# Kernel tuning notes

Measured on AMD Instinct MI355X. Metric: run time of the kernel, lower is better.

Reference implementation:

```python
import jax, jax.numpy as jnp
import numpy as np

BS, L, D = 2048, 32, 768
KS = 5  # gaussian kernel size
EPS = 1e-5


def layer_norm(x, g, b):
    m = x.mean(-1, keepdims=True)
    var = ((x - m) ** 2).mean(-1, keepdims=True)
    return (x - m) * jax.lax.rsqrt(var + EPS) * g + b


def setup_inputs() -> dict:
    key = jax.random.key(0)
    ks = jax.random.split(key, 12)
    s = 0.02
    return {
        "v": jax.random.normal(ks[0], (BS, L, D), jnp.float32),
        "qa": jax.random.normal(ks[1], (BS, D), jnp.float32),
        # v_proj: LayerNorm -> Linear(D,D) -> GELU
        "vp_lng": jnp.ones((D,), jnp.float32),
        "vp_lnb": jnp.zeros((D,), jnp.float32),
        "vp_w": jax.random.normal(ks[2], (D, D), jnp.float32) * s,
        "vp_b": jnp.zeros((D,), jnp.float32),
        # qa_proj: LayerNorm -> Linear(D,D) -> GELU
        "qp_lng": jnp.ones((D,), jnp.float32),
        "qp_lnb": jnp.zeros((D,), jnp.float32),
        "qp_w": jax.random.normal(ks[3], (D, D), jnp.float32) * s,
        "qp_b": jnp.zeros((D,), jnp.float32),
        # grounding: LayerNorm -> Linear(D,D/2) -> GELU -> Linear(D/2,1) -> Softmax(dim=-2)
        "g_lng": jnp.ones((D,), jnp.float32),
        "g_lnb": jnp.zeros((D,), jnp.float32),
        "g_w1": jax.random.normal(ks[4], (D, D // 2), jnp.float32) * s,
        "g_b1": jnp.zeros((D // 2,), jnp.float32),
        "g_w2": jax.random.normal(ks[5], (D // 2, 1), jnp.float32) * s,
        "g_b2": jnp.zeros((1,), jnp.float32),
        # adaptive gaussian filter sigma (scalar parameter, initial 1.0)
        "sigma": jnp.array(1.0, jnp.float32),
    }


def reference(v, qa, vp_lng, vp_lnb, vp_w, vp_b, qp_lng, qp_lnb, qp_w, qp_b,
              g_lng, g_lnb, g_w1, g_b1, g_w2, g_b2, sigma):
    bs, length = v.shape[0], v.shape[1]
    # projections (exact erf GELU, matching torch nn.GELU default)
    v_p = jax.nn.gelu(layer_norm(v, vp_lng, vp_lnb) @ vp_w + vp_b, approximate=False)
    qa_p = jax.nn.gelu(layer_norm(qa, qp_lng, qp_lnb) @ qp_w + qp_b, approximate=False)
    # gate = tanh(v @ qa) : [bs, L, 1]
    gate = jnp.tanh(jnp.einsum('bld,bd->bl', v_p, qa_p))[..., None]
    # grounding head -> softmax over frames
    h = layer_norm(v_p * gate, g_lng, g_lnb)
    h = jax.nn.gelu(h @ g_w1 + g_b1, approximate=False)
    logits = h @ g_w2 + g_b2                      # [bs, L, 1]
    ori_key = jax.nn.softmax(logits, axis=1)[..., 0]  # [bs, L]
    # adaptive gaussian smoothing (depthwise conv1d, symmetric 5-tap kernel) + softmax
    xk = jnp.arange(KS, dtype=jnp.float32) - KS // 2
    kern = jnp.exp(-0.5 * (xk / sigma) ** 2)
    kern = kern / kern.sum()
    xp = jnp.pad(ori_key, ((0, 0), (KS // 2, KS // 2)))
    taps = jnp.stack([xp[:, k:k + length] for k in range(KS)], axis=0)  # [KS, bs, L]
    smoothed = jnp.einsum('k,kbl->bl', kern, taps)
    key_gs = jax.nn.softmax(smoothed, axis=1)         # [bs, L]
    # find_best_interval_v2, vectorized: among windows of size {1,3,5} that
    # contain the (first) argmax frame, pick the window with highest prob-sum;
    # ties resolve to smallest window then earliest start (strict > in loop ==
    # first occurrence of the max in (w, start) order == jnp.argmax semantics).
    pmax = jnp.argmax(key_gs, axis=1)                 # [bs]
    cum = jnp.pad(jnp.cumsum(key_gs, axis=1), ((0, 0), (1, 0)))
    scores_all, starts_all, ends_all = [], [], []
    for w in (1, 3, 5):
        s = jnp.arange(length - w + 1)
        sums = cum[:, s + w] - cum[:, s]              # sliding window sums
        contains = (pmax[:, None] >= s[None, :]) & (pmax[:, None] < s[None, :] + w)
        scores_all.append(jnp.where(contains, sums, -jnp.inf))
        starts_all.append(s)
        ends_all.append(s + w)                        # NOTE: exclusive end stored, as in original
    scores = jnp.concatenate(scores_all, axis=1)
    starts = jnp.concatenate(starts_all)
    ends = jnp.concatenate(ends_all)
    idx = jnp.argmax(scores, axis=1)
    st = starts[idx]
    en = ends[idx]
    max_indices = jnp.stack([st, en], axis=1)         # [bs, 2]
    rng = jnp.arange(length)
    mask = (rng[None, :] >= st[:, None]) & (rng[None, :] <= en[:, None])
    start_time = st.astype(jnp.float32) / 31.0
    end_time = en.astype(jnp.float32) / 31.0
    return key_gs, max_indices, start_time, end_time, mask, ori_key
```

## Files before the change

kernel.cpp:

```cpp
#include <hip/hip_runtime.h>
#include <math.h>
#include <stdint.h>


#define DEV __device__ __forceinline__

typedef __attribute__((ext_vector_type(8))) short short8v;
typedef __attribute__((ext_vector_type(4))) float f32x4;

constexpr int KDIM  = 768;
constexpr int CHUNK = 32768;

constexpr int OFF_KG   = 0;
constexpr int OFF_MI   = 65536;
constexpr int OFF_ST   = 69632;
constexpr int OFF_ET   = 71680;
constexpr int OFF_MASK = 73728;
constexpr int OFF_ORI  = 139264;

DEV float wave_sum(float v) { for (int o = 32; o; o >>= 1) v += __shfl_xor(v, o); return v; }
DEV float wave_max(float v) { for (int o = 32; o; o >>= 1) v = fmaxf(v, __shfl_xor(v, o)); return v; }

DEV float gelu_fast(float x) {
    float z = x * 0.70710678118654752f;
    float s = fabsf(z);
    float t = __builtin_amdgcn_rcpf(fmaf(0.3275911f, s, 1.0f));
    float p = t * fmaf(t, fmaf(t, fmaf(t, fmaf(t, 1.061405429f, -1.453152027f),
                                       1.421413741f), -0.284496736f), 0.254829592f);
    float e = __expf(-s * s);
    float er = copysignf(1.0f - p * e, z);
    return 0.5f * x * (1.0f + er);
}

DEV short f2bf(float x) {
    uint32_t u = __builtin_bit_cast(uint32_t, x);
    u = u + 0x7fffu + ((u >> 16) & 1u);
    return (short)(u >> 16);
}
DEV float bf2f(short b) {
    uint32_t u = ((uint32_t)(uint16_t)b) << 16;
    return __builtin_bit_cast(float, u);
}
DEV float asf(uint32_t u) { return __builtin_bit_cast(float, u); }

DEV void gl_lds16(const void* g, void* l) {
    __builtin_amdgcn_global_load_lds(
        (const __attribute__((address_space(1))) uint32_t*)g,
        (__attribute__((address_space(3))) uint32_t*)l, 16, 0, 0);
}

__global__ __launch_bounds__(256)
void prep_A1(const float* __restrict__ X, const float* __restrict__ g,
             const float* __restrict__ b, short* __restrict__ Ah, short* __restrict__ Al)
{
    int w = threadIdx.x >> 6, lane = threadIdx.x & 63;
    int row = blockIdx.x * 4 + w;
    const float4* xr = (const float4*)(X + (size_t)row * KDIM);
    float4 xv[3]; float s = 0.f, ss = 0.f;
#pragma unroll
    for (int i = 0; i < 3; ++i) {
        xv[i] = xr[lane + i * 64];
        s  += xv[i].x + xv[i].y + xv[i].z + xv[i].w;
        ss += xv[i].x * xv[i].x + xv[i].y * xv[i].y + xv[i].z * xv[i].z + xv[i].w * xv[i].w;
    }
    s = wave_sum(s); ss = wave_sum(ss);
    float m = s * (1.f / 768.f), var = ss * (1.f / 768.f) - m * m;
    float sa = rsqrtf(var + 1e-5f), ta = -m * sa;
#pragma unroll
    for (int i = 0; i < 3; ++i) {
        int idx = lane + i * 64;
        float4 gv = ((const float4*)g)[idx];
        float4 bv = ((const float4*)b)[idx];
        float a0 = fmaf(fmaf(xv[i].x, sa, ta), gv.x, bv.x);
        float a1 = fmaf(fmaf(xv[i].y, sa, ta), gv.y, bv.y);
        float a2 = fmaf(fmaf(xv[i].z, sa, ta), gv.z, bv.z);
        float a3 = fmaf(fmaf(xv[i].w, sa, ta), gv.w, bv.w);
        short h0 = f2bf(a0), h1 = f2bf(a1), h2 = f2bf(a2), h3 = f2bf(a3);
        ushort4 hv, lv;
        hv.x = (uint16_t)h0; hv.y = (uint16_t)h1; hv.z = (uint16_t)h2; hv.w = (uint16_t)h3;
        lv.x = (uint16_t)f2bf(a0 - bf2f(h0)); lv.y = (uint16_t)f2bf(a1 - bf2f(h1));
        lv.z = (uint16_t)f2bf(a2 - bf2f(h2)); lv.w = (uint16_t)f2bf(a3 - bf2f(h3));
        ((ushort4*)(Ah + (size_t)row * KDIM))[idx] = hv;
        ((ushort4*)(Al + (size_t)row * KDIM))[idx] = lv;
    }
}

__global__ __launch_bounds__(256)
void prep_W(const float* __restrict__ W, const float* __restrict__ scale,
            short* __restrict__ Bh, short* __restrict__ Bl, int N)
{
    __shared__ float t[32][33];
    int bx = blockIdx.x, by = blockIdx.y;
    int lx = threadIdx.x & 31, ly = threadIdx.x >> 5;
#pragma unroll
    for (int r = 0; r < 32; r += 8)
        t[ly + r][lx] = W[(size_t)(by * 32 + ly + r) * N + bx * 32 + lx];
    __syncthreads();
    float sc = scale ? scale[by * 32 + lx] : 1.0f;
#pragma unroll
    for (int r = 0; r < 32; r += 8) {
        float v = t[lx][ly + r] * sc;
        short hi = f2bf(v);
        size_t o = (size_t)(bx * 32 + ly + r) * KDIM + by * 32 + lx;
        Bh[o] = hi;
        Bl[o] = f2bf(v - bf2f(hi));
    }
}

__global__ __launch_bounds__(256)
void colsums(const float* __restrict__ W1, const float* __restrict__ g2,
             const float* __restrict__ lb2, const float* __restrict__ b1,
             float* __restrict__ c1, float* __restrict__ c2)
{
    int w = threadIdx.x >> 6, lane = threadIdx.x & 63;
    int n = blockIdx.x * 4 + w;
    float s1 = 0.f, s2 = 0.f;
    for (int k = lane; k < 768; k += 64) {
        float wv = W1[(size_t)k * 384 + n];
        s1 += g2[k] * wv;
        s2 += lb2[k] * wv;
    }
    s1 = wave_sum(s1); s2 = wave_sum(s2);
    if (lane == 0) { c1[n] = s1; c2[n] = b1[n] + s2; }
}

__global__ __launch_bounds__(256)
void stats2(const float* __restrict__ sums, float2* __restrict__ st2, int chunk_off)
{
    int r = chunk_off + blockIdx.x * 256 + threadIdx.x;
    float s = 0.f, ss = 0.f, d = 0.f;
#pragma unroll
    for (int p = 0; p < 8; ++p) {
        s  += sums[(size_t)(0 * 8 + p) * 65536 + r];
        ss += sums[(size_t)(1 * 8 + p) * 65536 + r];
        d  += sums[(size_t)(2 * 8 + p) * 65536 + r];
    }
    float gate = tanhf(d);
    float m = s * (1.f / 768.f), var = ss * (1.f / 768.f) - m * m;
    float den = rsqrtf(gate * gate * var + 1e-5f);
    st2[r] = make_float2(gate * den, -gate * m * den);
}

#define VMW(N_) asm volatile("s_waitcnt vmcnt(" #N_ ")" ::: "memory")
#define SCB __builtin_amdgcn_sched_barrier(0)

#define STG(G_, KT_) gl_lds16(sp[G_] + (KT_) * 32,                            \
    lds + (((KT_) & 1) ? BUFSZ : 0) + (G_) * 4096 + toff)

#define STGA10(KT_) do { STG(0, KT_); STG(1, KT_); STG(2, KT_); STG(3, KT_);  \
    STG(4, KT_); STG(5, KT_); STG(6, KT_); STG(7, KT_); STG(8, KT_);          \
    STG(9, KT_); } while (0)

#define RDA(dst, BOFF) do { _Pragma("unroll")                                 \
    for (int mf = 0; mf < 4; ++mf) {                                          \
        int rA = wm * 64 + mf * 16 + lr;                                      \
        dst[mf] = *(const short8v*)(bb + (BOFF) + rA * 64 +                   \
                                    ((lh ^ ((rA >> 1) & 3)) << 4));           \
    } } while (0)

#define RDB(dst, BOFF) do { _Pragma("unroll")                                 \
    for (int nf = 0; nf < 6; ++nf) {                                          \
        int rB = wn * 96 + nf * 16 + lr;                                      \
        dst[nf] = *(const short8v*)(bb + (BOFF) + rB * 64 +                   \
                                    ((lh ^ ((rB >> 1) & 3)) << 4));           \
    } } while (0)

#define BODY(KT_, NL_) do {                                                   \
    if (NL_) { STGA10((KT_) + 1); }                                           \
    SCB;                                                                      \
    if (NL_) { VMW(10); } else { VMW(0); }                                    \
    SCB;                                                                      \
    __builtin_amdgcn_s_barrier();                \
    const char* bb = lds + (((KT_) & 1) ? BUFSZ : 0);                         \
    RDA(ah, 0); RDA(al, 8192); RDB(bh, 16384); RDB(bl, 28672);                \
    asm volatile("s_waitcnt lgkmcnt(0)" ::: "memory");                        \
    SCB;                                                                      \
    __builtin_amdgcn_s_barrier();                     \
    __builtin_amdgcn_s_setprio(1);                                            \
    _Pragma("unroll")                                                         \
    for (int mf = 0; mf < 4; ++mf)                                            \
        _Pragma("unroll")                                                     \
        for (int nf = 0; nf < 6; ++nf) {                                      \
            acc[mf][nf] = __builtin_amdgcn_mfma_f32_16x16x32_bf16(            \
                ah[mf], bh[nf], acc[mf][nf], 0, 0, 0);                        \
            acc[mf][nf] = __builtin_amdgcn_mfma_f32_16x16x32_bf16(            \
                ah[mf], bl[nf], acc[mf][nf], 0, 0, 0);                        \
            acc[mf][nf] = __builtin_amdgcn_mfma_f32_16x16x32_bf16(            \
                al[mf], bh[nf], acc[mf][nf], 0, 0, 0);                        \
        }                                                                     \
    __builtin_amdgcn_s_setprio(0);                                            \
    SCB;                                                                      \
} while (0)

template<int MODE>
__global__ __launch_bounds__(256, 2)
void gemm8(const short* __restrict__ Ah_g, const short* __restrict__ Al_g,
           const short* __restrict__ Bh_g, const short* __restrict__ Bl_g,
           const float* __restrict__ bias,
           short* __restrict__ Oh, short* __restrict__ Ol,
           const float* __restrict__ qa_p, float* __restrict__ sums,
           const float2* __restrict__ st2, const float* __restrict__ c1,
           const float* __restrict__ c2, const float* __restrict__ w2,
           float* __restrict__ partials, int chunk_off)
{
    constexpr int BUFSZ = 40960;
    extern __shared__ __align__(16) char lds[];

    const int t = threadIdx.x;
    const int w = t >> 6, lane = t & 63;
    const int lr = lane & 15, lh = lane >> 4;
    const int wm = w >> 1, wn = w & 1;

    const int gx = gridDim.x, nwg = gx * gridDim.y;
    int bidx = blockIdx.y * gx + blockIdx.x;
    int wid = (bidx & 7) * (nwg >> 3) + (bidx >> 3);
    const int bx = wid % gx, by = wid / gx;
    const int row0 = by * 128, col0 = bx * 192;

    const int r_ = t >> 2, c_ = t & 3;
    const int swz_ = (c_ ^ ((r_ >> 1) & 3)) << 3;
    const int toff = t * 16;
    const short* sp[10];
    sp[0] = Ah_g + (size_t)(row0 + r_)       * KDIM + swz_;
    sp[1] = Ah_g + (size_t)(row0 + 64 + r_)  * KDIM + swz_;
    sp[2] = Al_g + (size_t)(row0 + r_)       * KDIM + swz_;
    sp[3] = Al_g + (size_t)(row0 + 64 + r_)  * KDIM + swz_;
    sp[4] = Bh_g + (size_t)(col0 + r_)       * KDIM + swz_;
    sp[5] = Bh_g + (size_t)(col0 + 64 + r_)  * KDIM + swz_;
    sp[6] = Bh_g + (size_t)(col0 + 128 + r_) * KDIM + swz_;
    sp[7] = Bl_g + (size_t)(col0 + r_)       * KDIM + swz_;
    sp[8] = Bl_g + (size_t)(col0 + 64 + r_)  * KDIM + swz_;
    sp[9] = Bl_g + (size_t)(col0 + 128 + r_) * KDIM + swz_;

    f32x4 acc[4][6] = {};
    short8v ah[4], al[4], bh[6], bl[6];

    STGA10(0);
    SCB;

    for (int kt = 0; kt < 24; kt += 2) {
        BODY(kt,     true);
        BODY(kt + 1, (kt + 1 < 23));
    }

    if (MODE == 0) {
        __syncthreads();
        float* qal = (float*)lds;
        int bbase = (chunk_off >> 5) + (row0 >> 5);
        for (int j = t; j < 768; j += 256)
            qal[j] = qa_p[(size_t)(bbase + j / 192) * 768 + col0 + (j % 192)];
        __syncthreads();
#pragma unroll
        for (int mf = 0; mf < 4; ++mf) {
            const int bp = wm * 2 + (mf >> 1);
#pragma unroll
            for (int q = 0; q < 4; ++q) {
                int m = row0 + wm * 64 + mf * 16 + lh * 4 + q;
                float s = 0.f, ssq = 0.f, d = 0.f;
#pragma unroll
                for (int nf = 0; nf < 6; ++nf) {
                    int ncol = wn * 96 + nf * 16 + lr;
                    int n = col0 + ncol;
                    float gv = gelu_fast(acc[mf][nf][q] + bias[n]);
                    uint32_t u  = __builtin_bit_cast(uint32_t, gv);
                    uint32_t hb = u & 0xffff0000u;
                    float rem   = gv - asf(hb);
                    Oh[(size_t)m * 768 + n] = (short)(hb >> 16);
                    Ol[(size_t)m * 768 + n] = f2bf(rem);
                    s += gv; ssq += gv * gv; d += gv * qal[bp * 192 + ncol];
                }
                for (int o = 1; o < 16; o <<= 1) {
                    s += __shfl_xor(s, o); ssq += __shfl_xor(ssq, o); d += __shfl_xor(d, o);
                }
                if (lr == 0) {
                    int gr = chunk_off + m;
                    int pc = bx * 2 + wn;
                    sums[(size_t)(0 * 8 + pc) * 65536 + gr] = s;
                    sums[(size_t)(1 * 8 + pc) * 65536 + gr] = ssq;
                    sums[(size_t)(2 * 8 + pc) * 65536 + gr] = d;
                }
            }
        }
    } else {
        float c1v[6], c2v[6], wv[6];
#pragma unroll
        for (int nf = 0; nf < 6; ++nf) {
            int n = col0 + wn * 96 + nf * 16 + lr;
            c1v[nf] = c1[n]; c2v[nf] = c2[n]; wv[nf] = w2[n];
        }
        float rs[4][4] = {};
#pragma unroll
        for (int mf = 0; mf < 4; ++mf)
#pragma unroll
            for (int q = 0; q < 4; ++q) {
                int gm = chunk_off + row0 + wm * 64 + mf * 16 + lh * 4 + q;
                float2 st = st2[gm];
#pragma unroll
                for (int nf = 0; nf < 6; ++nf) {
                    float h = fmaf(st.x, acc[mf][nf][q], fmaf(st.y, c1v[nf], c2v[nf]));
                    rs[mf][q] += gelu_fast(h) * wv[nf];
                }
            }
#pragma unroll
        for (int mf = 0; mf < 4; ++mf)
#pragma unroll
            for (int q = 0; q < 4; ++q) {
                float vv = rs[mf][q];
                vv += __shfl_xor(vv, 1); vv += __shfl_xor(vv, 2);
                vv += __shfl_xor(vv, 4); vv += __shfl_xor(vv, 8);
                if (lr == 0) {
                    int gm = chunk_off + row0 + wm * 64 + mf * 16 + lh * 4 + q;
                    partials[(size_t)(bx * 2 + wn) * 65536 + gm] = vv;
                }
            }
    }
}

constexpr int BKF = 16;
__global__ __launch_bounds__(256)
void rowstats(const float* __restrict__ X, float2* __restrict__ st, int M)
{
    int wave = threadIdx.x >> 6, lane = threadIdx.x & 63;
    int row = blockIdx.x * 4 + wave;
    if (row >= M) return;
    const float4* xr = reinterpret_cast<const float4*>(X + (size_t)row * KDIM);
    float s = 0.f, ss = 0.f;
#pragma unroll
    for (int i = 0; i < 3; ++i) {
        float4 v = xr[lane + i * 64];
        s  += v.x + v.y + v.z + v.w;
        ss += v.x * v.x + v.y * v.y + v.z * v.z + v.w * v.w;
    }
    s = wave_sum(s); ss = wave_sum(ss);
    if (lane == 0) {
        float m = s * (1.0f / 768.0f);
        float var = ss * (1.0f / 768.0f) - m * m;
        float rstd = rsqrtf(var + 1e-5f);
        st[row] = make_float2(rstd, -m * rstd);
    }
}

template<int BM, int BN, int TM, int TN>
__global__ __launch_bounds__(256)
void gemm_fused(const float* __restrict__ X, const float2* __restrict__ st,
                const float* __restrict__ gw, const float* __restrict__ gb,
                const float* __restrict__ W, const float* __restrict__ bias,
                float* __restrict__ out, int M, int N)
{
    static_assert((BM / TM) * (BN / TN) == 256, "256 threads");
    __shared__ float As[BKF][BM];
    __shared__ float Bs[BKF][BN];
    const int t = threadIdx.x;
    constexpr int TXN = BN / TN;
    const int tx = t % TXN;
    const int ty = t / TXN;
    const int row0 = blockIdx.y * BM;
    const int col0 = blockIdx.x * BN;
    float acc[TM][TN] = {};
    constexpr int A_IT = BM * BKF / 4 / 256;
    constexpr int B_IT = BKF * BN / 4 / 256;
    for (int k0 = 0; k0 < KDIM; k0 += BKF) {
#pragma unroll
        for (int i = 0; i < A_IT; ++i) {
            int idx = t + i * 256;
            int r = idx >> 2;
            int c = (idx & 3) << 2;
            float4 xv = *reinterpret_cast<const float4*>(X + (size_t)(row0 + r) * KDIM + k0 + c);
            float2 s = st[row0 + r];
            float4 gv = *reinterpret_cast<const float4*>(gw + k0 + c);
            float4 bv = *reinterpret_cast<const float4*>(gb + k0 + c);
            As[c + 0][r] = fmaf(fmaf(xv.x, s.x, s.y), gv.x, bv.x);
            As[c + 1][r] = fmaf(fmaf(xv.y, s.x, s.y), gv.y, bv.y);
            As[c + 2][r] = fmaf(fmaf(xv.z, s.x, s.y), gv.z, bv.z);
            As[c + 3][r] = fmaf(fmaf(xv.w, s.x, s.y), gv.w, bv.w);
        }
#pragma unroll
        for (int i = 0; i < B_IT; ++i) {
            int idx = t + i * 256;
            int r = idx / (BN / 4);
            int c = (idx % (BN / 4)) << 2;
            *reinterpret_cast<float4*>(&Bs[r][c]) =
                *reinterpret_cast<const float4*>(W + (size_t)(k0 + r) * N + col0 + c);
        }
        __syncthreads();
#pragma unroll
        for (int kk = 0; kk < BKF; ++kk) {
            float a[TM], b[TN];
#pragma unroll
            for (int i = 0; i < TM; i += 4)
                *reinterpret_cast<float4*>(&a[i]) = *reinterpret_cast<const float4*>(&As[kk][ty * TM + i]);
#pragma unroll
            for (int j = 0; j < TN; j += 4)
                *reinterpret_cast<float4*>(&b[j]) = *reinterpret_cast<const float4*>(&Bs[kk][tx * TN + j]);
#pragma unroll
            for (int i = 0; i < TM; ++i)
#pragma unroll
                for (int j = 0; j < TN; ++j)
                    acc[i][j] = fmaf(a[i], b[j], acc[i][j]);
        }
        __syncthreads();
    }
#pragma unroll
    for (int i = 0; i < TM; ++i) {
        size_t row = row0 + ty * TM + i;
#pragma unroll
        for (int j = 0; j < TN; j += 4) {
            int col = col0 + tx * TN + j;
            float4 o;
            o.x = gelu_fast(acc[i][j + 0] + bias[col + 0]);
            o.y = gelu_fast(acc[i][j + 1] + bias[col + 1]);
            o.z = gelu_fast(acc[i][j + 2] + bias[col + 2]);
            o.w = gelu_fast(acc[i][j + 3] + bias[col + 3]);
            *reinterpret_cast<float4*>(out + row * N + col) = o;
        }
    }
}

__global__ __launch_bounds__(64)
void head_kernel(const float* __restrict__ partials, const float* __restrict__ b2,
                 const float* __restrict__ sigma_p, float* __restrict__ out)
{
    int b = blockIdx.x, lane = threadIdx.x;
    __shared__ float ok[36];
    __shared__ float kg[32];
    __shared__ int sel[2];

    if (lane < 36) ok[lane] = 0.f;
    __syncthreads();

    float x = -3.4e38f;
    if (lane < 32) {
        int row = b * 32 + lane;
        x = b2[0];
#pragma unroll
        for (int p = 0; p < 4; ++p) x += partials[(size_t)p * 65536 + row];
    }
    float mx = wave_max(x);
    float e = (lane < 32) ? expf(x - mx) : 0.f;
    float sum = wave_sum(e);
    float ori = e / sum;
    if (lane < 32) {
        out[OFF_ORI + b * 32 + lane] = ori;
        ok[lane + 2] = ori;
    }
    __syncthreads();

    float sg = sigma_p[0];
    float kern[5]; float ks = 0.f;
#pragma unroll
    for (int k = 0; k < 5; ++k) { float xx = (float)(k - 2) / sg; kern[k] = expf(-0.5f * xx * xx); ks += kern[k]; }
    float sm = -3.4e38f;
    if (lane < 32) {
        sm = 0.f;
#pragma unroll
        for (int k = 0; k < 5; ++k) sm += (kern[k] / ks) * ok[lane + k];
    }
    float mx2 = wave_max(sm);
    float e2 = (lane < 32) ? expf(sm - mx2) : 0.f;
    float sum2 = wave_sum(e2);
    float kgv = e2 / sum2;
    if (lane < 32) {
        out[OFF_KG + b * 32 + lane] = kgv;
        kg[lane] = kgv;
    }
    __syncthreads();

    if (lane == 0) {
        int pm = 0; float bv = kg[0];
        for (int i = 1; i < 32; ++i) if (kg[i] > bv) { bv = kg[i]; pm = i; }
        float cum[33]; cum[0] = 0.f;
        for (int i = 0; i < 32; ++i) cum[i + 1] = cum[i] + kg[i];
        float bs = -3.4e38f; int bst = 0, ben = 0;
        const int wsz[3] = {1, 3, 5};
        for (int wi = 0; wi < 3; ++wi) {
            int w = wsz[wi];
            for (int s = 0; s + w <= 32; ++s) {
                if (pm >= s && pm < s + w) {
                    float sc = cum[s + w] - cum[s];
                    if (sc > bs) { bs = sc; bst = s; ben = s + w; }
                }
            }
        }
        out[OFF_MI + b * 2 + 0] = (float)bst;
        out[OFF_MI + b * 2 + 1] = (float)ben;
        out[OFF_ST + b] = (float)bst / 31.0f;
        out[OFF_ET + b] = (float)ben / 31.0f;
        sel[0] = bst; sel[1] = ben;
    }
    __syncthreads();
    if (lane < 32)
        out[OFF_MASK + b * 32 + lane] = (lane >= sel[0] && lane <= sel[1]) ? 1.0f : 0.0f;
}

extern "C" void kernel_launch(void* const* d_in, const int* in_sizes, int n_in,
                              void* d_out, int out_size, void* d_ws, size_t ws_size,
                              hipStream_t stream)
{
    const float* v      = (const float*)d_in[0];
    const float* qa     = (const float*)d_in[1];
    const float* vp_lng = (const float*)d_in[2];
    const float* vp_lnb = (const float*)d_in[3];
    const float* vp_w   = (const float*)d_in[4];
    const float* vp_b   = (const float*)d_in[5];
    const float* qp_lng = (const float*)d_in[6];
    const float* qp_lnb = (const float*)d_in[7];
    const float* qp_w   = (const float*)d_in[8];
    const float* qp_b   = (const float*)d_in[9];
    const float* g_lng  = (const float*)d_in[10];
    const float* g_lnb  = (const float*)d_in[11];
    const float* g_w1   = (const float*)d_in[12];
    const float* g_b1   = (const float*)d_in[13];
    const float* g_w2   = (const float*)d_in[14];
    const float* g_b2   = (const float*)d_in[15];
    const float* sigma  = (const float*)d_in[16];
    float* outf = (float*)d_out;

    short* A1h = (short*)d_ws;
    short* A1l = A1h + (size_t)CHUNK * KDIM;
    short* vph = A1l + (size_t)CHUNK * KDIM;
    short* vpl = vph + (size_t)CHUNK * KDIM;
    short* B1h = vpl + (size_t)CHUNK * KDIM;
    short* B1l = B1h + 768 * KDIM;
    short* B2h = B1l + 768 * KDIM;
    short* B2l = B2h + 384 * KDIM;
    float* qa_p = (float*)(B2l + 384 * KDIM);
    float* st_qa = qa_p + 2048 * KDIM;
    float* partials = st_qa + 4096;
    float* sums = partials + 4 * 65536;
    float2* st2 = (float2*)(sums + 24 * 65536);
    float* c1 = (float*)(st2 + 65536);
    float* c2 = c1 + 384;

    rowstats<<<512, 256, 0, stream>>>(qa, (float2*)st_qa, 2048);
    gemm_fused<64, 64, 4, 4><<<dim3(12, 32), 256, 0, stream>>>(
        qa, (const float2*)st_qa, qp_lng, qp_lnb, qp_w, qp_b, qa_p, 2048, 768);

    prep_W<<<dim3(24, 24), 256, 0, stream>>>(vp_w, nullptr, B1h, B1l, 768);
    prep_W<<<dim3(12, 24), 256, 0, stream>>>(g_w1, g_lng, B2h, B2l, 384);
    colsums<<<96, 256, 0, stream>>>(g_w1, g_lng, g_lnb, g_b1, c1, c2);

    constexpr int LDS8 = 81920;

    for (int c = 0; c < 65536; c += CHUNK) {
        prep_A1<<<CHUNK / 4, 256, 0, stream>>>(v + (size_t)c * KDIM, vp_lng, vp_lnb, A1h, A1l);
        gemm8<0><<<dim3(4, CHUNK / 128), 256, LDS8, stream>>>(
            A1h, A1l, B1h, B1l, vp_b, vph, vpl, qa_p, sums,
            nullptr, nullptr, nullptr, nullptr, nullptr, c);
        stats2<<<CHUNK / 256, 256, 0, stream>>>(sums, st2, c);
        gemm8<1><<<dim3(2, CHUNK / 128), 256, LDS8, stream>>>(
            vph, vpl, B2h, B2l, nullptr, nullptr, nullptr, nullptr, nullptr,
            (const float2*)st2, c1, c2, g_w2, partials, c);
    }

    head_kernel<<<2048, 64, 0, stream>>>(partials, g_b2, sigma, outf);
}
```

Baseline: 517.3 us.

## Interleave bf16 hi/lo split of A operands into packed 32-bit words

Stores the activations' bf16 high and low halves together as one packed uint32 per element, replacing two separate short arrays. This applies to the LayerNorm prep output and to the first GEMM's GELU output that feeds the second GEMM. The GEMM staging now loads A rows from a single interleaved buffer with a new XOR swizzle, then unpacks hi and lo fragments in registers with shifts and masks before the MFMAs. The intent is fewer, wider global stores and contiguous A loads. The cost is extra ALU unpack work in the inner loop and a changed LDS bank pattern.

```diff
diff --git a/kernel.cpp b/kernel.cpp
--- a/kernel.cpp
+++ b/kernel.cpp
@@ -7,6 +7,7 @@
 
 typedef __attribute__((ext_vector_type(8))) short short8v;
 typedef __attribute__((ext_vector_type(4))) float f32x4;
+typedef __attribute__((ext_vector_type(4))) uint32_t u32x4;
 
 constexpr int KDIM  = 768;
 constexpr int CHUNK = 32768;
@@ -43,15 +44,36 @@
 }
 DEV float asf(uint32_t u) { return __builtin_bit_cast(float, u); }
 
+DEV uint32_t packhl(float x) {
+    uint32_t u  = __builtin_bit_cast(uint32_t, x);
+    uint32_t hb = u & 0xffff0000u;
+    float rem   = x - asf(hb);
+    return hb | (uint32_t)(uint16_t)f2bf(rem);
+}
+
 DEV void gl_lds16(const void* g, void* l) {
     __builtin_amdgcn_global_load_lds(
         (const __attribute__((address_space(1))) uint32_t*)g,
         (__attribute__((address_space(3))) uint32_t*)l, 16, 0, 0);
 }
 
+DEV void unpack8(u32x4 p0, u32x4 p1, short8v& hi, short8v& lo) {
+    u32x4 h, l;
+    h.x = (p0.x >> 16) | (p0.y & 0xffff0000u);
+    h.y = (p0.z >> 16) | (p0.w & 0xffff0000u);
+    h.z = (p1.x >> 16) | (p1.y & 0xffff0000u);
+    h.w = (p1.z >> 16) | (p1.w & 0xffff0000u);
+    l.x = (p0.x & 0xffffu) | (p0.y << 16);
+    l.y = (p0.z & 0xffffu) | (p0.w << 16);
+    l.z = (p1.x & 0xffffu) | (p1.y << 16);
+    l.w = (p1.z & 0xffffu) | (p1.w << 16);
+    hi = __builtin_bit_cast(short8v, h);
+    lo = __builtin_bit_cast(short8v, l);
+}
+
 __global__ __launch_bounds__(256)
 void prep_A1(const float* __restrict__ X, const float* __restrict__ g,
-             const float* __restrict__ b, short* __restrict__ Ah, short* __restrict__ Al)
+             const float* __restrict__ b, uint32_t* __restrict__ Ap)
 {
     int w = threadIdx.x >> 6, lane = threadIdx.x & 63;
     int row = blockIdx.x * 4 + w;
@@ -71,17 +93,12 @@
         int idx = lane + i * 64;
         float4 gv = ((const float4*)g)[idx];
         float4 bv = ((const float4*)b)[idx];
-        float a0 = fmaf(fmaf(xv[i].x, sa, ta), gv.x, bv.x);
-        float a1 = fmaf(fmaf(xv[i].y, sa, ta), gv.y, bv.y);
-        float a2 = fmaf(fmaf(xv[i].z, sa, ta), gv.z, bv.z);
-        float a3 = fmaf(fmaf(xv[i].w, sa, ta), gv.w, bv.w);
-        short h0 = f2bf(a0), h1 = f2bf(a1), h2 = f2bf(a2), h3 = f2bf(a3);
-        ushort4 hv, lv;
-        hv.x = (uint16_t)h0; hv.y = (uint16_t)h1; hv.z = (uint16_t)h2; hv.w = (uint16_t)h3;
-        lv.x = (uint16_t)f2bf(a0 - bf2f(h0)); lv.y = (uint16_t)f2bf(a1 - bf2f(h1));
-        lv.z = (uint16_t)f2bf(a2 - bf2f(h2)); lv.w = (uint16_t)f2bf(a3 - bf2f(h3));
-        ((ushort4*)(Ah + (size_t)row * KDIM))[idx] = hv;
-        ((ushort4*)(Al + (size_t)row * KDIM))[idx] = lv;
+        uint4 ov;
+        ov.x = packhl(fmaf(fmaf(xv[i].x, sa, ta), gv.x, bv.x));
+        ov.y = packhl(fmaf(fmaf(xv[i].y, sa, ta), gv.y, bv.y));
+        ov.z = packhl(fmaf(fmaf(xv[i].z, sa, ta), gv.z, bv.z));
+        ov.w = packhl(fmaf(fmaf(xv[i].w, sa, ta), gv.w, bv.w));
+        ((uint4*)(Ap + (size_t)row * KDIM))[idx] = ov;
     }
 }
 
@@ -144,18 +161,23 @@
 #define VMW(N_) asm volatile("s_waitcnt vmcnt(" #N_ ")" ::: "memory")
 #define SCB __builtin_amdgcn_sched_barrier(0)
 
-#define STG(G_, KT_) gl_lds16(sp[G_] + (KT_) * 32,                            \
-    lds + (((KT_) & 1) ? BUFSZ : 0) + (G_) * 4096 + toff)
-
-#define STGA10(KT_) do { STG(0, KT_); STG(1, KT_); STG(2, KT_); STG(3, KT_);  \
-    STG(4, KT_); STG(5, KT_); STG(6, KT_); STG(7, KT_); STG(8, KT_);          \
-    STG(9, KT_); } while (0)
-
-#define RDA(dst, BOFF) do { _Pragma("unroll")                                 \
+#define STGA(U_, KT_) gl_lds16(spA[U_] + (KT_) * 32,                          \
+    lds + (((KT_) & 1) ? BUFSZ : 0) + (U_) * 4096 + toff)
+#define STGB(J_, KT_) gl_lds16(spB[J_] + (KT_) * 32,                          \
+    lds + (((KT_) & 1) ? BUFSZ : 0) + 16384 + (J_) * 4096 + toff)
+
+#define STGALL(KT_) do { STGA(0, KT_); STGA(1, KT_); STGA(2, KT_);            \
+    STGA(3, KT_); STGB(0, KT_); STGB(1, KT_); STGB(2, KT_); STGB(3, KT_);     \
+    STGB(4, KT_); STGB(5, KT_); } while (0)
+
+#define RDAP do { _Pragma("unroll")                                           \
     for (int mf = 0; mf < 4; ++mf) {                                          \
         int rA = wm * 64 + mf * 16 + lr;                                      \
-        dst[mf] = *(const short8v*)(bb + (BOFF) + rA * 64 +                   \
-                                    ((lh ^ ((rA >> 1) & 3)) << 4));           \
+        const char* pr = bb + rA * 128;                                       \
+        int x_ = rA & 7;                                                      \
+        u32x4 p0 = *(const u32x4*)(pr + (((2 * lh) ^ x_) << 4));              \
+        u32x4 p1 = *(const u32x4*)(pr + (((2 * lh + 1) ^ x_) << 4));          \
+        unpack8(p0, p1, ah[mf], al[mf]);                                      \
     } } while (0)
 
 #define RDB(dst, BOFF) do { _Pragma("unroll")                                 \
@@ -166,13 +188,13 @@
     } } while (0)
 
 #define BODY(KT_, NL_) do {                                                   \
-    if (NL_) { STGA10((KT_) + 1); }                                           \
+    if (NL_) { STGALL((KT_) + 1); }                                           \
     SCB;                                                                      \
     if (NL_) { VMW(10); } else { VMW(0); }                                    \
     SCB;                                                                      \
     __builtin_amdgcn_s_barrier();                \
     const char* bb = lds + (((KT_) & 1) ? BUFSZ : 0);                         \
-    RDA(ah, 0); RDA(al, 8192); RDB(bh, 16384); RDB(bl, 28672);                \
+    RDAP; RDB(bh, 16384); RDB(bl, 28672);                                     \
     asm volatile("s_waitcnt lgkmcnt(0)" ::: "memory");                        \
     SCB;                                                                      \
     __builtin_amdgcn_s_barrier();                     \
@@ -194,10 +216,9 @@
 
 template<int MODE>
 __global__ __launch_bounds__(256, 2)
-void gemm8(const short* __restrict__ Ah_g, const short* __restrict__ Al_g,
+void gemm8(const uint32_t* __restrict__ Ap_g,
            const short* __restrict__ Bh_g, const short* __restrict__ Bl_g,
-           const float* __restrict__ bias,
-           short* __restrict__ Oh, short* __restrict__ Ol,
+           const float* __restrict__ bias, uint32_t* __restrict__ O_hl,
            const float* __restrict__ qa_p, float* __restrict__ sums,
            const float2* __restrict__ st2, const float* __restrict__ c1,
            const float* __restrict__ c2, const float* __restrict__ w2,
@@ -217,25 +238,28 @@
     const int bx = wid % gx, by = wid / gx;
     const int row0 = by * 128, col0 = bx * 192;
 
-    const int r_ = t >> 2, c_ = t & 3;
-    const int swz_ = (c_ ^ ((r_ >> 1) & 3)) << 3;
+    const int rA_ = t >> 3, cA_ = t & 7;
+    const uint32_t* spA[4];
+#pragma unroll
+    for (int u = 0; u < 4; ++u)
+        spA[u] = Ap_g + (size_t)(row0 + u * 32 + rA_) * KDIM
+                      + ((cA_ ^ (rA_ & 7)) << 2);
+    const int rB_ = t >> 2, cB_ = t & 3;
+    const int swzB = (cB_ ^ ((rB_ >> 1) & 3)) << 3;
+    const short* spB[6];
+    spB[0] = Bh_g + (size_t)(col0 + rB_)       * KDIM + swzB;
+    spB[1] = Bh_g + (size_t)(col0 + 64 + rB_)  * KDIM + swzB;
+    spB[2] = Bh_g + (size_t)(col0 + 128 + rB_) * KDIM + swzB;
+    spB[3] = Bl_g + (size_t)(col0 + rB_)       * KDIM + swzB;
+    spB[4] = Bl_g + (size_t)(col0 + 64 + rB_)  * KDIM + swzB;
+    spB[5] = Bl_g + (size_t)(col0 + 128 + rB_) * KDIM + swzB;
+
     const int toff = t * 16;
-    const short* sp[10];
-    sp[0] = Ah_g + (size_t)(row0 + r_)       * KDIM + swz_;
-    sp[1] = Ah_g + (size_t)(row0 + 64 + r_)  * KDIM + swz_;
-    sp[2] = Al_g + (size_t)(row0 + r_)       * KDIM + swz_;
-    sp[3] = Al_g + (size_t)(row0 + 64 + r_)  * KDIM + swz_;
-    sp[4] = Bh_g + (size_t)(col0 + r_)       * KDIM + swz_;
-    sp[5] = Bh_g + (size_t)(col0 + 64 + r_)  * KDIM + swz_;
-    sp[6] = Bh_g + (size_t)(col0 + 128 + r_) * KDIM + swz_;
-    sp[7] = Bl_g + (size_t)(col0 + r_)       * KDIM + swz_;
-    sp[8] = Bl_g + (size_t)(col0 + 64 + r_)  * KDIM + swz_;
-    sp[9] = Bl_g + (size_t)(col0 + 128 + r_) * KDIM + swz_;
 
     f32x4 acc[4][6] = {};
     short8v ah[4], al[4], bh[6], bl[6];
 
-    STGA10(0);
+    STGALL(0);
     SCB;
 
     for (int kt = 0; kt < 24; kt += 2) {
@@ -262,11 +286,7 @@
                     int ncol = wn * 96 + nf * 16 + lr;
                     int n = col0 + ncol;
                     float gv = gelu_fast(acc[mf][nf][q] + bias[n]);
-                    uint32_t u  = __builtin_bit_cast(uint32_t, gv);
-                    uint32_t hb = u & 0xffff0000u;
-                    float rem   = gv - asf(hb);
-                    Oh[(size_t)m * 768 + n] = (short)(hb >> 16);
-                    Ol[(size_t)m * 768 + n] = f2bf(rem);
+                    O_hl[(size_t)m * 768 + n] = packhl(gv);
                     s += gv; ssq += gv * gv; d += gv * qal[bp * 192 + ncol];
                 }
                 for (int o = 1; o < 16; o <<= 1) {
@@ -515,11 +535,9 @@
     const float* sigma  = (const float*)d_in[16];
     float* outf = (float*)d_out;
 
-    short* A1h = (short*)d_ws;
-    short* A1l = A1h + (size_t)CHUNK * KDIM;
-    short* vph = A1l + (size_t)CHUNK * KDIM;
-    short* vpl = vph + (size_t)CHUNK * KDIM;
-    short* B1h = vpl + (size_t)CHUNK * KDIM;
+    uint32_t* A1p = (uint32_t*)d_ws;
+    uint32_t* vp_hl = A1p + (size_t)CHUNK * KDIM;
+    short* B1h = (short*)(vp_hl + (size_t)CHUNK * KDIM);
     short* B1l = B1h + 768 * KDIM;
     short* B2h = B1l + 768 * KDIM;
     short* B2l = B2h + 384 * KDIM;
@@ -542,13 +560,13 @@
     constexpr int LDS8 = 81920;
 
     for (int c = 0; c < 65536; c += CHUNK) {
-        prep_A1<<<CHUNK / 4, 256, 0, stream>>>(v + (size_t)c * KDIM, vp_lng, vp_lnb, A1h, A1l);
+        prep_A1<<<CHUNK / 4, 256, 0, stream>>>(v + (size_t)c * KDIM, vp_lng, vp_lnb, A1p);
         gemm8<0><<<dim3(4, CHUNK / 128), 256, LDS8, stream>>>(
-            A1h, A1l, B1h, B1l, vp_b, vph, vpl, qa_p, sums,
+            A1p, B1h, B1l, vp_b, vp_hl, qa_p, sums,
             nullptr, nullptr, nullptr, nullptr, nullptr, c);
         stats2<<<CHUNK / 256, 256, 0, stream>>>(sums, st2, c);
         gemm8<1><<<dim3(2, CHUNK / 128), 256, LDS8, stream>>>(
-            vph, vpl, B2h, B2l, nullptr, nullptr, nullptr, nullptr, nullptr,
+            vp_hl, B2h, B2l, nullptr, nullptr, nullptr, nullptr,
             (const float2*)st2, c1, c2, g_w2, partials, c);
     }
 
```

Measured after the change: 516.0 us. Within noise of the previous version (-0.3%).
